# Kernel optimization log

Hardware: AMD Instinct MI355X
Metric: run time of the kernel (lower is better)

The kernel has to match this reference:

```python
import jax, jax.numpy as jnp
import numpy as np

N_NODES = 100000
N_EDGES = 1600000
D_FEAT = 64
EPS = 1e-07


def setup_inputs() -> dict:
    key = jax.random.key(0)
    k1, k2, k3 = jax.random.split(key, 3)
    x = jax.random.normal(k1, (N_NODES, D_FEAT), dtype=jnp.float32)
    beta = jnp.ones((1,), dtype=jnp.float32)
    edge_row = jnp.sort(jax.random.randint(k2, (N_EDGES,), 0, N_NODES, dtype=jnp.int64))
    edge_col = jax.random.randint(k3, (N_EDGES,), 0, N_NODES, dtype=jnp.int64)
    return {"x": x, "beta": beta, "edge_row": edge_row, "edge_col": edge_col}


def reference(x, beta, edge_row, edge_col):
    # Gather endpoint features: [E, d]
    A = x[edge_row]
    B = x[edge_col]
    # Cosine similarity per edge, scaled by beta: [E]
    inner = jnp.sum(A * B, axis=1)
    norms = jnp.linalg.norm(A, axis=1) * jnp.linalg.norm(B, axis=1)
    sim = beta[0] * (inner / (norms + EPS))
    # Sparse row-wise softmax (tf.sparse.softmax): stable segment softmax over edges grouped by row
    row_max = jax.ops.segment_max(sim, edge_row, num_segments=N_NODES)
    e = jnp.exp(sim - row_max[edge_row])
    row_sum = jax.ops.segment_sum(e, edge_row, num_segments=N_NODES)
    p = e / row_sum[edge_row]  # [E]
    # SPMM: out[i] = sum_{(i,j) in E} p_ij * x[j]
    out = jax.ops.segment_sum(p[:, None] * B, edge_row, num_segments=N_NODES)
    return out
```

## Files before the change

kernel.cpp:

```cpp
#include <hip/hip_runtime.h>
#include <math.h>

#define D_FEAT 64
typedef _Float16 v8h __attribute__((ext_vector_type(8)));
typedef float v4f __attribute__((ext_vector_type(4)));
typedef _Float16 h2 __attribute__((ext_vector_type(2)));

__device__ __forceinline__ v8h u2h8(uint4 u) { v8h v; __builtin_memcpy(&v, &u, 16); return v; }

__global__ __launch_bounds__(256)
void agnn_prep(const float* __restrict__ x, float* __restrict__ rn,
               uint2* __restrict__ xh, const int* __restrict__ edge_row,
               int* __restrict__ row_ptr, int n_nodes, int n_edges, int nb_prep) {
    if ((int)blockIdx.x < nb_prep) {
        int t = blockIdx.x * blockDim.x + threadIdx.x;
        int node = t >> 4;
        if (node >= n_nodes) return;
        int l4 = t & 15;
        float4 v = ((const float4*)x)[node * 16 + l4];
        float ss = v.x*v.x + v.y*v.y + v.z*v.z + v.w*v.w;
        #pragma unroll
        for (int off = 1; off < 16; off <<= 1) ss += __shfl_xor(ss, off, 64);
        if (l4 == 0) rn[node] = ss > 0.f ? rsqrtf(ss) : 0.f;
        h2 h0 = {(_Float16)v.x, (_Float16)v.y};
        h2 h1 = {(_Float16)v.z, (_Float16)v.w};
        uint2 u;
        __builtin_memcpy(&u.x, &h0, 4);
        __builtin_memcpy(&u.y, &h1, 4);
        xh[node * 16 + l4] = u;
    } else {
        int e = (blockIdx.x - nb_prep) * blockDim.x + threadIdx.x;
        if (e >= n_edges) return;
        int r1 = edge_row[e];
        int r0 = (e == 0) ? -1 : edge_row[e - 1];
        for (int r = r0 + 1; r <= r1; ++r) row_ptr[r] = e;
        if (e == n_edges - 1)
            for (int r = r1 + 1; r <= n_nodes; ++r) row_ptr[r] = n_edges;
    }
}

#define XCP_PITCH 144
#define P_PITCH    80
#define WAVE_LDS  (32 * XCP_PITCH + 16 * P_PITCH)

__global__ __launch_bounds__(128)
void agnn_fused(const float* __restrict__ beta_p,
                const int* __restrict__ edge_col,
                const int* __restrict__ row_ptr,
                const float* __restrict__ rn,
                const uint4* __restrict__ xh4,
                float* __restrict__ out, int n_nodes) {
    __shared__ char lds_raw[2 * WAVE_LDS];
    int wid  = threadIdx.x >> 6;
    int lane = threadIdx.x & 63;
    int q    = lane >> 4;
    int lo4  = lane & 15;
    char* XCP = lds_raw + wid * WAVE_LDS;
    char* PL  = XCP + 32 * XCP_PITCH;

    int tile = blockIdx.x;
    int t0 = tile * 16;

    int qnode = t0 + lo4; if (qnode >= n_nodes) qnode = n_nodes - 1;
    v8h a0 = u2h8(xh4[(size_t)qnode * 8 + q]);
    v8h a1 = u2h8(xh4[(size_t)qnode * 8 + 4 + q]);

    float beta  = beta_p[0];
    float shift = fabsf(beta);
    int rb = t0 + q * 4;
    float brn0, brn1, brn2, brn3;
    if (t0 + 16 <= n_nodes) {
        float4 rq = *(const float4*)(rn + rb);
        brn0 = beta * rq.x; brn1 = beta * rq.y; brn2 = beta * rq.z; brn3 = beta * rq.w;
    } else {
        brn0 = beta * rn[min(rb + 0, n_nodes - 1)];
        brn1 = beta * rn[min(rb + 1, n_nodes - 1)];
        brn2 = beta * rn[min(rb + 2, n_nodes - 1)];
        brn3 = beta * rn[min(rb + 3, n_nodes - 1)];
    }

    int es   = row_ptr[t0];
    int tend = t0 + 16; if (tend > n_nodes) tend = n_nodes;
    int L    = row_ptr[tend] - es;

    int b0 = row_ptr[min(rb + 0, n_nodes)] - es;
    int b1 = row_ptr[min(rb + 1, n_nodes)] - es;
    int b2 = row_ptr[min(rb + 2, n_nodes)] - es;
    int b3 = row_ptr[min(rb + 3, n_nodes)] - es;
    int b4 = row_ptr[min(rb + 4, n_nodes)] - es;

    v4f o0 = {0,0,0,0}, o1 = {0,0,0,0}, o2 = {0,0,0,0}, o3 = {0,0,0,0};
    float l0 = 0.f, l1 = 0.f, l2 = 0.f, l3 = 0.f;
    unsigned int selp = (lo4 & 1) ? 0x07060302u : 0x05040100u;

    int nch  = (L + 31) >> 5;
    int nchw = (nch > wid) ? ((nch - wid + 1) >> 1) : 0;
    if (nchw > 0) {
        int cc0, cc1;
        {
            int i0 = (wid << 5) + lo4, i1 = i0 + 16;
            cc0 = edge_col[es + (i0 < L ? i0 : 0)];
            cc1 = edge_col[es + (i1 < L ? i1 : 0)];
        }
        float rc0 = rn[cc0], rc1 = rn[cc1];
        uint4 A00 = xh4[(size_t)cc0 * 8 + q];
        uint4 A01 = xh4[(size_t)cc0 * 8 + 4 + q];
        uint4 A10 = xh4[(size_t)cc1 * 8 + q];
        uint4 A11 = xh4[(size_t)cc1 * 8 + 4 + q];

        for (int k = 0; k < nchw; ++k) {
            int base = (wid + 2 * k) << 5;
            bool more = (k + 1) < nchw;

            int nc0, nc1;
            if (more) {
                int i0 = base + 64 + lo4, i1 = i0 + 16;
                nc0 = edge_col[es + (i0 < L ? i0 : 0)];
                nc1 = edge_col[es + (i1 < L ? i1 : 0)];
            } else { nc0 = cc0; nc1 = cc1; }

            v4f z0 = {0,0,0,0};
            z0 = __builtin_amdgcn_mfma_f32_16x16x32_f16(a0, u2h8(A00), z0, 0, 0, 0);
            z0 = __builtin_amdgcn_mfma_f32_16x16x32_f16(a1, u2h8(A01), z0, 0, 0, 0);
            v4f z1 = {0,0,0,0};
            z1 = __builtin_amdgcn_mfma_f32_16x16x32_f16(a0, u2h8(A10), z1, 0, 0, 0);
            z1 = __builtin_amdgcn_mfma_f32_16x16x32_f16(a1, u2h8(A11), z1, 0, 0, 0);

            {
                unsigned int colA = lo4 * 4, colB = (16 + lo4) * 4;
                char* pA = XCP + (4 * q) * XCP_PITCH;
                char* pB = XCP + (16 + 4 * q) * XCP_PITCH;
                *(unsigned int*)(pA + 0 * XCP_PITCH + colA) = A00.x;
                *(unsigned int*)(pA + 1 * XCP_PITCH + colA) = A00.y;
                *(unsigned int*)(pA + 2 * XCP_PITCH + colA) = A00.z;
                *(unsigned int*)(pA + 3 * XCP_PITCH + colA) = A00.w;
                *(unsigned int*)(pB + 0 * XCP_PITCH + colA) = A01.x;
                *(unsigned int*)(pB + 1 * XCP_PITCH + colA) = A01.y;
                *(unsigned int*)(pB + 2 * XCP_PITCH + colA) = A01.z;
                *(unsigned int*)(pB + 3 * XCP_PITCH + colA) = A01.w;
                *(unsigned int*)(pA + 0 * XCP_PITCH + colB) = A10.x;
                *(unsigned int*)(pA + 1 * XCP_PITCH + colB) = A10.y;
                *(unsigned int*)(pA + 2 * XCP_PITCH + colB) = A10.z;
                *(unsigned int*)(pA + 3 * XCP_PITCH + colB) = A10.w;
                *(unsigned int*)(pB + 0 * XCP_PITCH + colB) = A11.x;
                *(unsigned int*)(pB + 1 * XCP_PITCH + colB) = A11.y;
                *(unsigned int*)(pB + 2 * XCP_PITCH + colB) = A11.z;
                *(unsigned int*)(pB + 3 * XCP_PITCH + colB) = A11.w;
            }

            float nr0, nr1; uint4 B00, B01, B10, B11;
            if (more) {
                nr0 = rn[nc0]; nr1 = rn[nc1];
                B00 = xh4[(size_t)nc0 * 8 + q];
                B01 = xh4[(size_t)nc0 * 8 + 4 + q];
                B10 = xh4[(size_t)nc1 * 8 + q];
                B11 = xh4[(size_t)nc1 * 8 + 4 + q];
            } else {
                nr0 = rc0; nr1 = rc1;
                B00 = A00; B01 = A01; B10 = A10; B11 = A11;
            }

            int i0g = base + lo4, i1g = i0g + 16;
            float w00 = (i0g >= b0 && i0g < b1) ? __expf(brn0 * rc0 * z0[0] - shift) : 0.f;
            float w01 = (i0g >= b1 && i0g < b2) ? __expf(brn1 * rc0 * z0[1] - shift) : 0.f;
            float w02 = (i0g >= b2 && i0g < b3) ? __expf(brn2 * rc0 * z0[2] - shift) : 0.f;
            float w03 = (i0g >= b3 && i0g < b4) ? __expf(brn3 * rc0 * z0[3] - shift) : 0.f;
            float w10 = (i1g >= b0 && i1g < b1) ? __expf(brn0 * rc1 * z1[0] - shift) : 0.f;
            float w11 = (i1g >= b1 && i1g < b2) ? __expf(brn1 * rc1 * z1[1] - shift) : 0.f;
            float w12 = (i1g >= b2 && i1g < b3) ? __expf(brn2 * rc1 * z1[2] - shift) : 0.f;
            float w13 = (i1g >= b3 && i1g < b4) ? __expf(brn3 * rc1 * z1[3] - shift) : 0.f;
            l0 += w00 + w10; l1 += w01 + w11; l2 += w02 + w12; l3 += w03 + w13;

            {
                unsigned int cA = lo4 * 2, cB = (16 + lo4) * 2;
                char* pm = PL + (q * 4) * P_PITCH;
                *(_Float16*)(pm + 0 * P_PITCH + cA) = (_Float16)w00;
                *(_Float16*)(pm + 1 * P_PITCH + cA) = (_Float16)w01;
                *(_Float16*)(pm + 2 * P_PITCH + cA) = (_Float16)w02;
                *(_Float16*)(pm + 3 * P_PITCH + cA) = (_Float16)w03;
                *(_Float16*)(pm + 0 * P_PITCH + cB) = (_Float16)w10;
                *(_Float16*)(pm + 1 * P_PITCH + cB) = (_Float16)w11;
                *(_Float16*)(pm + 2 * P_PITCH + cB) = (_Float16)w12;
                *(_Float16*)(pm + 3 * P_PITCH + cB) = (_Float16)w13;
            }

            v8h pah = u2h8(*(const uint4*)(PL + lo4 * P_PITCH + q * 16));
            {
                const char* rp = XCP + (0 + (lo4 >> 1)) * XCP_PITCH + q * 32;
                uint4 da = *(const uint4*)rp;
                uint4 db = *(const uint4*)(rp + 16);
                uint4 bb = { __builtin_amdgcn_perm(da.y, da.x, selp),
                             __builtin_amdgcn_perm(da.w, da.z, selp),
                             __builtin_amdgcn_perm(db.y, db.x, selp),
                             __builtin_amdgcn_perm(db.w, db.z, selp) };
                o0 = __builtin_amdgcn_mfma_f32_16x16x32_f16(pah, u2h8(bb), o0, 0, 0, 0);
            }
            {
                const char* rp = XCP + (8 + (lo4 >> 1)) * XCP_PITCH + q * 32;
                uint4 da = *(const uint4*)rp;
                uint4 db = *(const uint4*)(rp + 16);
                uint4 bb = { __builtin_amdgcn_perm(da.y, da.x, selp),
                             __builtin_amdgcn_perm(da.w, da.z, selp),
                             __builtin_amdgcn_perm(db.y, db.x, selp),
                             __builtin_amdgcn_perm(db.w, db.z, selp) };
                o1 = __builtin_amdgcn_mfma_f32_16x16x32_f16(pah, u2h8(bb), o1, 0, 0, 0);
            }
            {
                const char* rp = XCP + (16 + (lo4 >> 1)) * XCP_PITCH + q * 32;
                uint4 da = *(const uint4*)rp;
                uint4 db = *(const uint4*)(rp + 16);
                uint4 bb = { __builtin_amdgcn_perm(da.y, da.x, selp),
                             __builtin_amdgcn_perm(da.w, da.z, selp),
                             __builtin_amdgcn_perm(db.y, db.x, selp),
                             __builtin_amdgcn_perm(db.w, db.z, selp) };
                o2 = __builtin_amdgcn_mfma_f32_16x16x32_f16(pah, u2h8(bb), o2, 0, 0, 0);
            }
            {
                const char* rp = XCP + (24 + (lo4 >> 1)) * XCP_PITCH + q * 32;
                uint4 da = *(const uint4*)rp;
                uint4 db = *(const uint4*)(rp + 16);
                uint4 bb = { __builtin_amdgcn_perm(da.y, da.x, selp),
                             __builtin_amdgcn_perm(da.w, da.z, selp),
                             __builtin_amdgcn_perm(db.y, db.x, selp),
                             __builtin_amdgcn_perm(db.w, db.z, selp) };
                o3 = __builtin_amdgcn_mfma_f32_16x16x32_f16(pah, u2h8(bb), o3, 0, 0, 0);
            }

            cc0 = nc0; cc1 = nc1; rc0 = nr0; rc1 = nr1;
            A00 = B00; A01 = B01; A10 = B10; A11 = B11;
        }
    }

    if (wid == 1) {
        char* ST = XCP;
        *(v4f*)(ST + lane * 80 +  0) = o0;
        *(v4f*)(ST + lane * 80 + 16) = o1;
        *(v4f*)(ST + lane * 80 + 32) = o2;
        *(v4f*)(ST + lane * 80 + 48) = o3;
        float4 lv = {l0, l1, l2, l3};
        *(float4*)(ST + lane * 80 + 64) = lv;
    }
    __syncthreads();
    if (wid == 1) return;
    {
        const char* ST = lds_raw + WAVE_LDS;
        o0 += *(const v4f*)(ST + lane * 80 +  0);
        o1 += *(const v4f*)(ST + lane * 80 + 16);
        o2 += *(const v4f*)(ST + lane * 80 + 32);
        o3 += *(const v4f*)(ST + lane * 80 + 48);
        float4 lv = *(const float4*)(ST + lane * 80 + 64);
        l0 += lv.x; l1 += lv.y; l2 += lv.z; l3 += lv.w;
    }

    #pragma unroll
    for (int off = 1; off < 16; off <<= 1) {
        l0 += __shfl_xor(l0, off, 64);
        l1 += __shfl_xor(l1, off, 64);
        l2 += __shfl_xor(l2, off, 64);
        l3 += __shfl_xor(l3, off, 64);
    }
    float i0 = l0 > 0.f ? 1.f / l0 : 0.f;
    float i1 = l1 > 0.f ? 1.f / l1 : 0.f;
    float i2 = l2 > 0.f ? 1.f / l2 : 0.f;
    float i3 = l3 > 0.f ? 1.f / l3 : 0.f;

    int m0 = rb;
    if (m0 + 0 < n_nodes) { float* p = out + (size_t)(m0 + 0) * 64 + lo4;
        p[0] = o0[0]*i0; p[16] = o1[0]*i0; p[32] = o2[0]*i0; p[48] = o3[0]*i0; }
    if (m0 + 1 < n_nodes) { float* p = out + (size_t)(m0 + 1) * 64 + lo4;
        p[0] = o0[1]*i1; p[16] = o1[1]*i1; p[32] = o2[1]*i1; p[48] = o3[1]*i1; }
    if (m0 + 2 < n_nodes) { float* p = out + (size_t)(m0 + 2) * 64 + lo4;
        p[0] = o0[2]*i2; p[16] = o1[2]*i2; p[32] = o2[2]*i2; p[48] = o3[2]*i2; }
    if (m0 + 3 < n_nodes) { float* p = out + (size_t)(m0 + 3) * 64 + lo4;
        p[0] = o0[3]*i3; p[16] = o1[3]*i3; p[32] = o2[3]*i3; p[48] = o3[3]*i3; }
}

extern "C" void kernel_launch(void* const* d_in, const int* in_sizes, int n_in,
                              void* d_out, int out_size, void* d_ws, size_t ws_size,
                              hipStream_t stream) {
    const float* x        = (const float*)d_in[0];
    const float* beta     = (const float*)d_in[1];
    const int*   edge_row = (const int*)d_in[2];
    const int*   edge_col = (const int*)d_in[3];
    float* out = (float*)d_out;

    int n_nodes = in_sizes[0] / D_FEAT;
    int n_edges = in_sizes[2];

    char* ws = (char*)d_ws;
    float* rn = (float*)ws;
    size_t off0 = ((size_t)n_nodes * sizeof(float) + 255) & ~(size_t)255;
    int* row_ptr = (int*)(ws + off0);
    size_t off1 = off0 + (((size_t)(n_nodes + 1) * sizeof(int) + 255) & ~(size_t)255);
    uint2* xh = (uint2*)(ws + off1);

    {
        int nb_prep = (n_nodes * 16 + 255) / 256;
        int nb_rp   = (n_edges + 255) / 256;
        agnn_prep<<<nb_prep + nb_rp, 256, 0, stream>>>(
            x, rn, xh, edge_row, row_ptr, n_nodes, n_edges, nb_prep);
    }
    {
        int tiles = (n_nodes + 15) / 16;
        agnn_fused<<<tiles, 128, 0, stream>>>(beta, edge_col, row_ptr,
                                              rn, (const uint4*)xh, out, n_nodes);
    }
}
```

Measured before the change: 125.4 us.

## Transpose similarity MFMA and pass softmax weights via shuffles instead of LDS

Swaps the MFMA operands so the similarity tile comes out edge-major, which lets each lane own a single query row (one row_ptr bound pair, one beta*rn). The fp16 softmax weights are then packed and redistributed into the A-operand layout with cross-lane shuffles, instead of being written to and read back from a per-wave LDS P buffer. The row-sum reduction drops to two xor-shuffles. This removes LDS traffic and the P staging area, at the cost of about 20 extra shuffles per chunk. It also adds an early exit for tiles past n_nodes.

```diff
diff --git a/kernel.cpp b/kernel.cpp
--- a/kernel.cpp
+++ b/kernel.cpp
@@ -7,6 +7,10 @@
 typedef _Float16 h2 __attribute__((ext_vector_type(2)));
 
 __device__ __forceinline__ v8h u2h8(uint4 u) { v8h v; __builtin_memcpy(&v, &u, 16); return v; }
+__device__ __forceinline__ unsigned pkh(float a, float b) {
+    h2 r = {(_Float16)a, (_Float16)b};
+    unsigned u; __builtin_memcpy(&u, &r, 4); return u;
+}
 
 __global__ __launch_bounds__(256)
 void agnn_prep(const float* __restrict__ x, float* __restrict__ rn,
@@ -40,8 +44,7 @@
 }
 
 #define XCP_PITCH 144
-#define P_PITCH    80
-#define WAVE_LDS  (32 * XCP_PITCH + 16 * P_PITCH)
+#define WAVE_LDS  (32 * XCP_PITCH)
 
 __global__ __launch_bounds__(128)
 void agnn_fused(const float* __restrict__ beta_p,
@@ -56,10 +59,10 @@
     int q    = lane >> 4;
     int lo4  = lane & 15;
     char* XCP = lds_raw + wid * WAVE_LDS;
-    char* PL  = XCP + 32 * XCP_PITCH;
 
     int tile = blockIdx.x;
     int t0 = tile * 16;
+    if (t0 >= n_nodes) return;
 
     int qnode = t0 + lo4; if (qnode >= n_nodes) qnode = n_nodes - 1;
     v8h a0 = u2h8(xh4[(size_t)qnode * 8 + q]);
@@ -67,31 +70,18 @@
 
     float beta  = beta_p[0];
     float shift = fabsf(beta);
-    int rb = t0 + q * 4;
-    float brn0, brn1, brn2, brn3;
-    if (t0 + 16 <= n_nodes) {
-        float4 rq = *(const float4*)(rn + rb);
-        brn0 = beta * rq.x; brn1 = beta * rq.y; brn2 = beta * rq.z; brn3 = beta * rq.w;
-    } else {
-        brn0 = beta * rn[min(rb + 0, n_nodes - 1)];
-        brn1 = beta * rn[min(rb + 1, n_nodes - 1)];
-        brn2 = beta * rn[min(rb + 2, n_nodes - 1)];
-        brn3 = beta * rn[min(rb + 3, n_nodes - 1)];
-    }
-
+    float brn = beta * rn[qnode];
     int es   = row_ptr[t0];
     int tend = t0 + 16; if (tend > n_nodes) tend = n_nodes;
     int L    = row_ptr[tend] - es;
-
-    int b0 = row_ptr[min(rb + 0, n_nodes)] - es;
-    int b1 = row_ptr[min(rb + 1, n_nodes)] - es;
-    int b2 = row_ptr[min(rb + 2, n_nodes)] - es;
-    int b3 = row_ptr[min(rb + 3, n_nodes)] - es;
-    int b4 = row_ptr[min(rb + 4, n_nodes)] - es;
+    int blo  = row_ptr[min(t0 + lo4,     n_nodes)] - es;
+    int bhi  = row_ptr[min(t0 + lo4 + 1, n_nodes)] - es;
 
     v4f o0 = {0,0,0,0}, o1 = {0,0,0,0}, o2 = {0,0,0,0}, o3 = {0,0,0,0};
-    float l0 = 0.f, l1 = 0.f, l2 = 0.f, l3 = 0.f;
+    float lsum = 0.f;
     unsigned int selp = (lo4 & 1) ? 0x07060302u : 0x05040100u;
+    int srcA = ((q & 1) << 5) + lo4;
+    int srcB = srcA + 16;
 
     int nch  = (L + 31) >> 5;
     int nchw = (nch > wid) ? ((nch - wid + 1) >> 1) : 0;
@@ -120,11 +110,11 @@
             } else { nc0 = cc0; nc1 = cc1; }
 
             v4f z0 = {0,0,0,0};
-            z0 = __builtin_amdgcn_mfma_f32_16x16x32_f16(a0, u2h8(A00), z0, 0, 0, 0);
-            z0 = __builtin_amdgcn_mfma_f32_16x16x32_f16(a1, u2h8(A01), z0, 0, 0, 0);
+            z0 = __builtin_amdgcn_mfma_f32_16x16x32_f16(u2h8(A00), a0, z0, 0, 0, 0);
+            z0 = __builtin_amdgcn_mfma_f32_16x16x32_f16(u2h8(A01), a1, z0, 0, 0, 0);
             v4f z1 = {0,0,0,0};
-            z1 = __builtin_amdgcn_mfma_f32_16x16x32_f16(a0, u2h8(A10), z1, 0, 0, 0);
-            z1 = __builtin_amdgcn_mfma_f32_16x16x32_f16(a1, u2h8(A11), z1, 0, 0, 0);
+            z1 = __builtin_amdgcn_mfma_f32_16x16x32_f16(u2h8(A10), a0, z1, 0, 0, 0);
+            z1 = __builtin_amdgcn_mfma_f32_16x16x32_f16(u2h8(A11), a1, z1, 0, 0, 0);
 
             {
                 unsigned int colA = lo4 * 4, colB = (16 + lo4) * 4;
@@ -160,31 +150,33 @@
                 B00 = A00; B01 = A01; B10 = A10; B11 = A11;
             }
 
-            int i0g = base + lo4, i1g = i0g + 16;
-            float w00 = (i0g >= b0 && i0g < b1) ? __expf(brn0 * rc0 * z0[0] - shift) : 0.f;
-            float w01 = (i0g >= b1 && i0g < b2) ? __expf(brn1 * rc0 * z0[1] - shift) : 0.f;
-            float w02 = (i0g >= b2 && i0g < b3) ? __expf(brn2 * rc0 * z0[2] - shift) : 0.f;
-            float w03 = (i0g >= b3 && i0g < b4) ? __expf(brn3 * rc0 * z0[3] - shift) : 0.f;
-            float w10 = (i1g >= b0 && i1g < b1) ? __expf(brn0 * rc1 * z1[0] - shift) : 0.f;
-            float w11 = (i1g >= b1 && i1g < b2) ? __expf(brn1 * rc1 * z1[1] - shift) : 0.f;
-            float w12 = (i1g >= b2 && i1g < b3) ? __expf(brn2 * rc1 * z1[2] - shift) : 0.f;
-            float w13 = (i1g >= b3 && i1g < b4) ? __expf(brn3 * rc1 * z1[3] - shift) : 0.f;
-            l0 += w00 + w10; l1 += w01 + w11; l2 += w02 + w12; l3 += w03 + w13;
-
-            {
-                unsigned int cA = lo4 * 2, cB = (16 + lo4) * 2;
-                char* pm = PL + (q * 4) * P_PITCH;
-                *(_Float16*)(pm + 0 * P_PITCH + cA) = (_Float16)w00;
-                *(_Float16*)(pm + 1 * P_PITCH + cA) = (_Float16)w01;
-                *(_Float16*)(pm + 2 * P_PITCH + cA) = (_Float16)w02;
-                *(_Float16*)(pm + 3 * P_PITCH + cA) = (_Float16)w03;
-                *(_Float16*)(pm + 0 * P_PITCH + cB) = (_Float16)w10;
-                *(_Float16*)(pm + 1 * P_PITCH + cB) = (_Float16)w11;
-                *(_Float16*)(pm + 2 * P_PITCH + cB) = (_Float16)w12;
-                *(_Float16*)(pm + 3 * P_PITCH + cB) = (_Float16)w13;
-            }
-
-            v8h pah = u2h8(*(const uint4*)(PL + lo4 * P_PITCH + q * 16));
+            float rA0 = __shfl(rc0, 4*q + 0), rA1 = __shfl(rc0, 4*q + 1);
+            float rA2 = __shfl(rc0, 4*q + 2), rA3 = __shfl(rc0, 4*q + 3);
+            float rB0 = __shfl(rc1, 4*q + 0), rB1 = __shfl(rc1, 4*q + 1);
+            float rB2 = __shfl(rc1, 4*q + 2), rB3 = __shfl(rc1, 4*q + 3);
+
+            int eA = base + 4 * q, eB = eA + 16;
+            float wA0 = (eA+0 >= blo && eA+0 < bhi) ? __expf(brn * rA0 * z0[0] - shift) : 0.f;
+            float wA1 = (eA+1 >= blo && eA+1 < bhi) ? __expf(brn * rA1 * z0[1] - shift) : 0.f;
+            float wA2 = (eA+2 >= blo && eA+2 < bhi) ? __expf(brn * rA2 * z0[2] - shift) : 0.f;
+            float wA3 = (eA+3 >= blo && eA+3 < bhi) ? __expf(brn * rA3 * z0[3] - shift) : 0.f;
+            float wB0 = (eB+0 >= blo && eB+0 < bhi) ? __expf(brn * rB0 * z1[0] - shift) : 0.f;
+            float wB1 = (eB+1 >= blo && eB+1 < bhi) ? __expf(brn * rB1 * z1[1] - shift) : 0.f;
+            float wB2 = (eB+2 >= blo && eB+2 < bhi) ? __expf(brn * rB2 * z1[2] - shift) : 0.f;
+            float wB3 = (eB+3 >= blo && eB+3 < bhi) ? __expf(brn * rB3 * z1[3] - shift) : 0.f;
+            lsum += ((wA0 + wA1) + (wA2 + wA3)) + ((wB0 + wB1) + (wB2 + wB3));
+
+            unsigned d0 = pkh(wA0, wA1), d1 = pkh(wA2, wA3);
+            unsigned e0 = pkh(wB0, wB1), e1 = pkh(wB2, wB3);
+            unsigned uA0 = __shfl((int)d0, srcA), uA1 = __shfl((int)d1, srcA);
+            unsigned uB0 = __shfl((int)d0, srcB), uB1 = __shfl((int)d1, srcB);
+            unsigned vA0 = __shfl((int)e0, srcA), vA1 = __shfl((int)e1, srcA);
+            unsigned vB0 = __shfl((int)e0, srcB), vB1 = __shfl((int)e1, srcB);
+            uint4 pu;
+            if (q < 2) { pu.x = uA0; pu.y = uA1; pu.z = uB0; pu.w = uB1; }
+            else       { pu.x = vA0; pu.y = vA1; pu.z = vB0; pu.w = vB1; }
+            v8h pah = u2h8(pu);
+
             {
                 const char* rp = XCP + (0 + (lo4 >> 1)) * XCP_PITCH + q * 32;
                 uint4 da = *(const uint4*)rp;
@@ -233,38 +225,32 @@
 
     if (wid == 1) {
         char* ST = XCP;
-        *(v4f*)(ST + lane * 80 +  0) = o0;
-        *(v4f*)(ST + lane * 80 + 16) = o1;
-        *(v4f*)(ST + lane * 80 + 32) = o2;
-        *(v4f*)(ST + lane * 80 + 48) = o3;
-        float4 lv = {l0, l1, l2, l3};
-        *(float4*)(ST + lane * 80 + 64) = lv;
+        *(v4f*)(ST + lane * 68 +  0) = o0;
+        *(v4f*)(ST + lane * 68 + 16) = o1;
+        *(v4f*)(ST + lane * 68 + 32) = o2;
+        *(v4f*)(ST + lane * 68 + 48) = o3;
+        *(float*)(ST + 64 * 68 + lane * 4) = lsum;
     }
     __syncthreads();
     if (wid == 1) return;
     {
         const char* ST = lds_raw + WAVE_LDS;
-        o0 += *(const v4f*)(ST + lane * 80 +  0);
-        o1 += *(const v4f*)(ST + lane * 80 + 16);
-        o2 += *(const v4f*)(ST + lane * 80 + 32);
-        o3 += *(const v4f*)(ST + lane * 80 + 48);
-        float4 lv = *(const float4*)(ST + lane * 80 + 64);
-        l0 += lv.x; l1 += lv.y; l2 += lv.z; l3 += lv.w;
-    }
-
-    #pragma unroll
-    for (int off = 1; off < 16; off <<= 1) {
-        l0 += __shfl_xor(l0, off, 64);
-        l1 += __shfl_xor(l1, off, 64);
-        l2 += __shfl_xor(l2, off, 64);
-        l3 += __shfl_xor(l3, off, 64);
-    }
-    float i0 = l0 > 0.f ? 1.f / l0 : 0.f;
-    float i1 = l1 > 0.f ? 1.f / l1 : 0.f;
-    float i2 = l2 > 0.f ? 1.f / l2 : 0.f;
-    float i3 = l3 > 0.f ? 1.f / l3 : 0.f;
-
-    int m0 = rb;
+        o0 += *(const v4f*)(ST + lane * 68 +  0);
+        o1 += *(const v4f*)(ST + lane * 68 + 16);
+        o2 += *(const v4f*)(ST + lane * 68 + 32);
+        o3 += *(const v4f*)(ST + lane * 68 + 48);
+        lsum += *(const float*)(ST + 64 * 68 + lane * 4);
+    }
+
+    lsum += __shfl_xor(lsum, 16, 64);
+    lsum += __shfl_xor(lsum, 32, 64);
+    float inv = lsum > 0.f ? 1.f / lsum : 0.f;
+    float i0 = __shfl(inv, 4*q + 0);
+    float i1 = __shfl(inv, 4*q + 1);
+    float i2 = __shfl(inv, 4*q + 2);
+    float i3 = __shfl(inv, 4*q + 3);
+
+    int m0 = t0 + q * 4;
     if (m0 + 0 < n_nodes) { float* p = out + (size_t)(m0 + 0) * 64 + lo4;
         p[0] = o0[0]*i0; p[16] = o1[0]*i0; p[32] = o2[0]*i0; p[48] = o3[0]*i0; }
     if (m0 + 1 < n_nodes) { float* p = out + (size_t)(m0 + 1) * 64 + lo4;
```

New measurement: 126.3 us. About the same (+0.7%).
